# Kernel optimization log

Hardware: AMD Instinct MI355X
Metric: run time of the kernel (lower is better)

## Reference

```python
import jax, jax.numpy as jnp
import numpy as np

B, L, C = 8, 2048, 512
R, H, DK = 256, 8, 64
MASK_NEG = -2.0**15 + 1.0


def setup_inputs() -> dict:
    key = jax.random.key(0)
    ks = jax.random.split(key, 9)
    s = 1.0 / np.sqrt(C)
    return {
        "qx": jax.random.normal(ks[0], (B, L, C), jnp.float32),
        "kx": jax.random.normal(ks[1], (B, L, C), jnp.float32),
        "vx": jax.random.normal(ks[2], (B, L, C), jnp.float32),
        "addLoss": jnp.zeros((), jnp.float32),
        "maskPAD": jnp.ones((B, L, L), jnp.bool_),
        "Wp": jax.random.normal(ks[3], (R, C), jnp.float32) * s,
        "WQ": jax.random.normal(ks[4], (H * DK, C), jnp.float32) * s,
        "WK": jax.random.normal(ks[5], (H * DK, C), jnp.float32) * s,
        "WV": jax.random.normal(ks[6], (H * DK, C), jnp.float32) * s,
        "WO": jax.random.normal(ks[7], (C, H * DK), jnp.float32) * (1.0 / np.sqrt(H * DK)),
    }


def reference(qx, kx, vx, addLoss, maskPAD, Wp, WQ, WK, WV, WO):
    # linearLevel == 'l1', dropout treated as identity (eval), training losses included
    b, l, c = qx.shape
    r = Wp.shape[0]
    offI = (1.0 - jnp.eye(r, dtype=qx.dtype))  # ones_minus_I, [r, r]

    pScore = jnp.einsum('blc,rc->blr', vx, Wp)                       # [B, L, r]
    pad = (maskPAD[:, 0] == 0)                                       # [B, L]
    pScore = jnp.where(pad[:, :, None], MASK_NEG, pScore)
    pAlpha = jnp.swapaxes(jax.nn.softmax(pScore, axis=-2), -1, -2)   # [B, r, L]
    pAlpha_ = jax.nn.softmax(pScore, axis=-1)                        # [B, L, r]

    addLoss = addLoss + jnp.mean((jnp.einsum('brl,bsl->brs', pAlpha, pAlpha) * offI) ** 2)

    qr = pAlpha @ qx                                                 # [B, r, C]
    kr = pAlpha @ kx
    vr = pAlpha @ vx

    queries = (qr @ WQ.T).reshape(b, r, H, DK).transpose(0, 2, 1, 3)  # [B, H, r, dk]
    keys = (kr @ WK.T).reshape(b, r, H, DK).transpose(0, 2, 1, 3)
    values = (vr @ WV.T).reshape(b, r, H, DK).transpose(0, 2, 1, 3)

    scores = jnp.einsum('bhrd,bhsd->bhrs', queries, keys) / jnp.asarray(np.sqrt(DK), qx.dtype)
    alpha = jax.nn.softmax(scores, axis=-1)                          # [B, H, r, r]
    addLoss = addLoss + jnp.mean(alpha * offI)

    z = alpha @ values                                               # [B, H, r, dk]
    z = z.transpose(0, 2, 1, 3).reshape(b, r, H * DK)
    z = z @ WO.T                                                     # [B, r, C]

    addLoss = addLoss + jnp.mean((jnp.einsum('blr,bls->brs', pAlpha_, pAlpha_) * offI) ** 2)
    z = pAlpha_ @ z                                                  # [B, L, C]
    return z, scores, addLoss
```

## Files before the change

### kernel.cpp

```cpp
#include <hip/hip_runtime.h>

#define B_  8
#define L_  2048
#define C_  512
#define R_  256
#define H_  8
#define DK_ 64
#define HD_ 512
#define MASK_NEG (-32767.0f)

typedef __attribute__((ext_vector_type(8))) short short8;
typedef __attribute__((ext_vector_type(8))) unsigned short ushort8;
typedef __attribute__((ext_vector_type(4))) unsigned short ushort4_t;
typedef __attribute__((ext_vector_type(4))) float f32x4;
typedef unsigned short u16;

__device__ inline u16 bf16_rne(float x) {
    unsigned u = __float_as_uint(x);
    return (u16)((u + 0x7FFFu + ((u >> 16) & 1u)) >> 16);
}
__device__ inline unsigned cvt_hl(float x) {
    u16 hh = bf16_rne(x);
    float hf = __uint_as_float(((unsigned)hh) << 16);
    u16 ll = bf16_rne(x - hf);
    return (unsigned)hh | ((unsigned)ll << 16);
}

struct Ptr3 { const void* p0; const void* p1; const void* p2; };

#define GLL16(g, l) __builtin_amdgcn_global_load_lds( \
    (const __attribute__((address_space(1))) void*)(g), \
    (__attribute__((address_space(3))) void*)(l), 16, 0, 0)

template<int BN, int AMODE, int BMODE, int EPI, bool TRIPLE, int NTERM = 3, int KSPLIT = 1>
__global__ __launch_bounds__(256) void gemm_pl(
    Ptr3 aH, Ptr3 aL, Ptr3 bH, Ptr3 bL, Ptr3 cH, Ptr3 cL,
    Ptr3 cT1, Ptr3 cT2, int ldct, long long csT,
    int K, int lda, int ldb, int ldc, int divz,
    long long ash, long long bsh, long long csh,
    long long asb, long long bsb, long long csb,
    long long ksa, long long ksb, long long ksc,
    float scale)
{
    constexpr int NF = BN / 32;
    constexpr int XA = (NTERM == 3) ? 64 : 1;
    constexpr int XB = (NTERM == 3) ? BN : 1;
    __shared__ u16 Ahs[64][40], Als[XA][40];
    __shared__ u16 Bhs[BN][40], Bls[XB][40];

    const int gx = gridDim.x, gy = gridDim.y;
    const int nwg = gx * gy * gridDim.z;
    int flat = blockIdx.x + gx * (blockIdx.y + gy * blockIdx.z);
    {
        int q = nwg >> 3;
        int xcd = flat & 7, idx = flat >> 3;
        flat = xcd * q + idx;
    }
    const int bx = flat % gx;
    const int by = (flat / gx) % gy;
    const int z  = flat / (gx * gy);

    const int zb = z / divz;
    const int rem = z - zb * divz;
    const int zh = rem / KSPLIT, ks = rem - zh * KSPLIT;
    const int Keff = K / KSPLIT;
    const void* avH = TRIPLE ? (zb == 0 ? aH.p0 : zb == 1 ? aH.p1 : aH.p2) : aH.p0;
    const void* avL = TRIPLE ? (zb == 0 ? aL.p0 : zb == 1 ? aL.p1 : aL.p2) : aL.p0;
    const void* bvH = TRIPLE ? (zb == 0 ? bH.p0 : zb == 1 ? bH.p1 : bH.p2) : bH.p0;
    const void* bvL = TRIPLE ? (zb == 0 ? bL.p0 : zb == 1 ? bL.p1 : bL.p2) : bL.p0;
    void* cvH = (void*)(TRIPLE ? (zb == 0 ? cH.p0 : zb == 1 ? cH.p1 : cH.p2) : cH.p0);
    void* cvL = (void*)(TRIPLE ? (zb == 0 ? cL.p0 : zb == 1 ? cL.p1 : cL.p2) : cL.p0);
    void* cvT1 = (void*)(TRIPLE ? (zb == 0 ? cT1.p0 : zb == 1 ? cT1.p1 : cT1.p2) : cT1.p0);
    void* cvT2 = (void*)(TRIPLE ? (zb == 0 ? cT2.p0 : zb == 1 ? cT2.p1 : cT2.p2) : cT2.p0);
    const long long ao = (TRIPLE ? 0 : (long long)zb * asb) + (long long)zh * ash + (long long)ks * ksa;
    const long long bo = (TRIPLE ? 0 : (long long)zb * bsb) + (long long)zh * bsh + (long long)ks * ksb;
    const long long co = (TRIPLE ? 0 : (long long)zb * csb) + (long long)zh * csh + (long long)ks * ksc;
    const long long coT = (long long)zh * csT;

    const u16*   AHg = (const u16*)avH + ao;
    const u16*   ALg = (const u16*)avL + ao;
    const u16*   BHg = (const u16*)bvH + bo;
    const u16*   BLg = (const u16*)bvL + bo;
    const float* Bfg = (const float*)bvH + bo;
    float* Cf  = (float*)cvH + co;
    u16*   CHg = (u16*)cvH + co;
    u16*   CLg = (u16*)cvL + co;

    const int m0 = by * 64, n0 = bx * BN;
    const int tid = threadIdx.x;
    const int lane = tid & 63, w = tid >> 6;
    const int wrow = (w >> 1) * 32, wcol = (w & 1) * (BN / 2);
    const int l15 = lane & 15, lg = lane >> 4;

    f32x4 zero = {0.f, 0.f, 0.f, 0.f};
    f32x4 acc[2][NF];
    #pragma unroll
    for (int mf = 0; mf < 2; ++mf)
        #pragma unroll
        for (int nf = 0; nf < NF; ++nf) acc[mf][nf] = zero;

    for (int k0 = 0; k0 < Keff; k0 += 32) {
        {
            int row = tid >> 2, kc = (tid & 3) << 3;
            long long off = (long long)(m0 + row) * lda + (k0 + kc);
            *(ushort8*)&Ahs[row][kc] = *(const ushort8*)(AHg + off);
            if constexpr (NTERM == 3)
                *(ushort8*)&Als[row][kc] = *(const ushort8*)(ALg + off);
        }
        if (BMODE == 0) {
            #pragma unroll
            for (int t = tid; t < BN * 4; t += 256) {
                int row = t >> 2, kc = (t & 3) << 3;
                long long off = (long long)(n0 + row) * ldb + (k0 + kc);
                *(ushort8*)&Bhs[row][kc] = *(const ushort8*)(BHg + off);
                if constexpr (NTERM == 3)
                    *(ushort8*)&Bls[row][kc] = *(const ushort8*)(BLg + off);
            }
        } else {
            #pragma unroll
            for (int t = tid; t < BN * 4; t += 256) {
                int row = t >> 2, kc = (t & 3) << 3;
                const float* s = Bfg + (long long)(n0 + row) * ldb + (k0 + kc);
                float4 v0 = *(const float4*)s, v1 = *(const float4*)(s + 4);
                unsigned p0 = cvt_hl(v0.x), p1 = cvt_hl(v0.y), p2 = cvt_hl(v0.z), p3 = cvt_hl(v0.w);
                unsigned p4 = cvt_hl(v1.x), p5 = cvt_hl(v1.y), p6 = cvt_hl(v1.z), p7 = cvt_hl(v1.w);
                ushort8 h, l;
                h[0]=(u16)p0; h[1]=(u16)p1; h[2]=(u16)p2; h[3]=(u16)p3;
                h[4]=(u16)p4; h[5]=(u16)p5; h[6]=(u16)p6; h[7]=(u16)p7;
                l[0]=(u16)(p0>>16); l[1]=(u16)(p1>>16); l[2]=(u16)(p2>>16); l[3]=(u16)(p3>>16);
                l[4]=(u16)(p4>>16); l[5]=(u16)(p5>>16); l[6]=(u16)(p6>>16); l[7]=(u16)(p7>>16);
                *(ushort8*)&Bhs[row][kc] = h;
                if constexpr (NTERM == 3)
                    *(ushort8*)&Bls[row][kc] = l;
            }
        }
        __syncthreads();

        short8 a_h[2], a_l[2];
        a_h[0] = *(const short8*)&Ahs[wrow +      l15][lg * 8];
        a_h[1] = *(const short8*)&Ahs[wrow + 16 + l15][lg * 8];
        if constexpr (NTERM == 3) {
            a_l[0] = *(const short8*)&Als[wrow +      l15][lg * 8];
            a_l[1] = *(const short8*)&Als[wrow + 16 + l15][lg * 8];
        }
        #pragma unroll
        for (int nf = 0; nf < NF; ++nf) {
            short8 b_h = *(const short8*)&Bhs[wcol + nf * 16 + l15][lg * 8];
            if constexpr (NTERM == 3) {
                short8 b_l = *(const short8*)&Bls[wcol + nf * 16 + l15][lg * 8];
                #pragma unroll
                for (int mf = 0; mf < 2; ++mf) {
                    acc[mf][nf] = __builtin_amdgcn_mfma_f32_16x16x32_bf16(a_h[mf], b_h, acc[mf][nf], 0, 0, 0);
                    acc[mf][nf] = __builtin_amdgcn_mfma_f32_16x16x32_bf16(a_h[mf], b_l, acc[mf][nf], 0, 0, 0);
                    acc[mf][nf] = __builtin_amdgcn_mfma_f32_16x16x32_bf16(a_l[mf], b_h, acc[mf][nf], 0, 0, 0);
                }
            } else {
                #pragma unroll
                for (int mf = 0; mf < 2; ++mf)
                    acc[mf][nf] = __builtin_amdgcn_mfma_f32_16x16x32_bf16(a_h[mf], b_h, acc[mf][nf], 0, 0, 0);
            }
        }
        __syncthreads();
    }

    #pragma unroll
    for (int mf = 0; mf < 2; ++mf)
        #pragma unroll
        for (int nf = 0; nf < NF; ++nf) {
            int row = m0 + wrow + mf * 16 + lg * 4;
            int col = n0 + wcol + nf * 16 + l15;
            if constexpr (EPI == 0 || EPI == 3) {
                #pragma unroll
                for (int j = 0; j < 4; ++j)
                    Cf[(long long)(row + j) * ldc + col] = acc[mf][nf][j] * scale;
                if constexpr (EPI == 3) {
                    float* CfT = (float*)cvT1 + coT;
                    float4 v = make_float4(acc[mf][nf][0] * scale, acc[mf][nf][1] * scale,
                                           acc[mf][nf][2] * scale, acc[mf][nf][3] * scale);
                    *(float4*)(CfT + (long long)col * ldct + row) = v;
                }
            } else {
                unsigned p[4];
                #pragma unroll
                for (int j = 0; j < 4; ++j) {
                    p[j] = cvt_hl(acc[mf][nf][j] * scale);
                    if constexpr (EPI != 5) {
                        CHg[(long long)(row + j) * ldc + col] = (u16)p[j];
                        CLg[(long long)(row + j) * ldc + col] = (u16)(p[j] >> 16);
                    }
                }
                if constexpr (EPI == 4 || EPI == 5) {
                    u16* CTH = (u16*)cvT1 + coT;
                    u16* CTL = (u16*)cvT2 + coT;
                    ushort4_t h, l;
                    #pragma unroll
                    for (int j = 0; j < 4; ++j) { h[j] = (u16)p[j]; l[j] = (u16)(p[j] >> 16); }
                    *(ushort4_t*)(CTH + (long long)col * ldct + row) = h;
                    *(ushort4_t*)(CTL + (long long)col * ldct + row) = l;
                }
            }
        }
}

template<int EPI, bool TRIPLE, int NTERM, int KSPLIT, bool TRIANG = false>
__global__ __launch_bounds__(256) void gemm_gll(
    Ptr3 aH, Ptr3 aL, Ptr3 bH, Ptr3 bL, Ptr3 cH, Ptr3 cL,
    Ptr3 cT1, Ptr3 cT2, int ldct, long long csT,
    int K, int lda, int ldb, int ldc, int divz,
    long long ash, long long bsh, long long csh,
    long long ksa, long long ksb, long long ksc,
    float scale)
{
    constexpr int XA = (NTERM == 3) ? 128 : 1;
    __shared__ u16 Ahs[2][128][32];
    __shared__ u16 Bhs[2][128][32];
    __shared__ u16 Als[XA][32], Bls[XA][32];

    const int gx = gridDim.x, gy = gridDim.y;
    const int nwg = gx * gy * gridDim.z;
    int flat = blockIdx.x + gx * (blockIdx.y + gy * blockIdx.z);
    {
        int q = nwg >> 3;
        int xcd = flat & 7, idx = flat >> 3;
        flat = xcd * q + idx;
    }
    const int bx = flat % gx;
    const int by = (flat / gx) % gy;
    const int z  = flat / (gx * gy);

    const int zb = z / divz;
    const int rem = z - zb * divz;
    const int zh = rem / KSPLIT, ks = rem - zh * KSPLIT;
    const int Keff = K / KSPLIT;
    const void* avH = TRIPLE ? (zb == 0 ? aH.p0 : zb == 1 ? aH.p1 : aH.p2) : aH.p0;
    const void* avL = TRIPLE ? (zb == 0 ? aL.p0 : zb == 1 ? aL.p1 : aL.p2) : aL.p0;
    const void* bvH = TRIPLE ? (zb == 0 ? bH.p0 : zb == 1 ? bH.p1 : bH.p2) : bH.p0;
    const void* bvL = TRIPLE ? (zb == 0 ? bL.p0 : zb == 1 ? bL.p1 : bL.p2) : bL.p0;
    void* cvH = (void*)(TRIPLE ? (zb == 0 ? cH.p0 : zb == 1 ? cH.p1 : cH.p2) : cH.p0);
    void* cvL = (void*)(TRIPLE ? (zb == 0 ? cL.p0 : zb == 1 ? cL.p1 : cL.p2) : cL.p0);
    void* cvT1 = (void*)(TRIPLE ? (zb == 0 ? cT1.p0 : zb == 1 ? cT1.p1 : cT1.p2) : cT1.p0);
    void* cvT2 = (void*)(TRIPLE ? (zb == 0 ? cT2.p0 : zb == 1 ? cT2.p1 : cT2.p2) : cT2.p0);
    const long long ao = (long long)zh * ash + (long long)ks * ksa;
    const long long bo = (long long)zh * bsh + (long long)ks * ksb;
    const long long co = (long long)zh * csh + (long long)ks * ksc;
    const long long coT = (long long)zh * csT;

    const u16* AHg = (const u16*)avH + ao;
    const u16* ALg = (const u16*)avL + ao;
    const u16* BHg = (const u16*)bvH + bo;
    const u16* BLg = (const u16*)bvL + bo;
    float* Cf  = (float*)cvH + co;
    u16*   CHg = (u16*)cvH + co;
    u16*   CLg = (u16*)cvL + co;

    int m0, n0;
    if constexpr (TRIANG) {
        m0 = (bx >= 1) ? 128 : 0;
        n0 = (bx == 2) ? 128 : 0;
    } else {
        m0 = by * 128; n0 = bx * 128;
    }
    const int tid = threadIdx.x;
    const int lane = tid & 63, w = tid >> 6;
    const int wrow = (w >> 1) * 64, wcol = (w & 1) * 64;
    const int l15 = lane & 15, lg = lane >> 4;

    f32x4 zero = {0.f, 0.f, 0.f, 0.f};
    f32x4 acc[4][4];
    #pragma unroll
    for (int mf = 0; mf < 4; ++mf)
        #pragma unroll
        for (int nf = 0; nf < 4; ++nf) acc[mf][nf] = zero;

    const int ric = lane >> 2;
    const int cc  = lane & 3;

    auto STAGE_HI = [&](int bufsel, int k0) {
        #pragma unroll
        for (int i = 0; i < 2; ++i) {
            int chunk = w * 2 + i;
            int row = chunk * 16 + ric;
            int gcol = ((cc ^ ((row >> 1) & 3)) << 3);
            GLL16(AHg + (long long)(m0 + row) * lda + (k0 + gcol), &Ahs[bufsel][chunk * 16][0]);
            GLL16(BHg + (long long)(n0 + row) * ldb + (k0 + gcol), &Bhs[bufsel][chunk * 16][0]);
        }
    };
    auto STAGE_LO = [&](int k0) {
        #pragma unroll
        for (int i = 0; i < 2; ++i) {
            int chunk = w * 2 + i;
            int row = chunk * 16 + ric;
            int gcol = ((cc ^ ((row >> 1) & 3)) << 3);
            GLL16(ALg + (long long)(m0 + row) * lda + (k0 + gcol), &Als[chunk * 16][0]);
            GLL16(BLg + (long long)(n0 + row) * ldb + (k0 + gcol), &Bls[chunk * 16][0]);
        }
    };

    const int nt = Keff / 32;
    int cur = 0;
    STAGE_HI(0, 0);

    for (int t = 0; t < nt; ++t) {
        if constexpr (NTERM == 3) STAGE_LO(t * 32);
        if (t + 1 < nt) {
            STAGE_HI(cur ^ 1, (t + 1) * 32);
            asm volatile("s_waitcnt vmcnt(4)" ::: "memory");
        } else {
            asm volatile("s_waitcnt vmcnt(0)" ::: "memory");
        }
        __builtin_amdgcn_s_barrier();

        short8 a_h[4], a_l[4];
        #pragma unroll
        for (int mf = 0; mf < 4; ++mf) {
            int ar = wrow + mf * 16 + l15;
            int ac = (lg ^ ((ar >> 1) & 3)) << 3;
            a_h[mf] = *(const short8*)&Ahs[cur][ar][ac];
            if constexpr (NTERM == 3) a_l[mf] = *(const short8*)&Als[ar][ac];
        }
        __builtin_amdgcn_s_setprio(1);
        #pragma unroll
        for (int nf = 0; nf < 4; ++nf) {
            int br = wcol + nf * 16 + l15;
            int bc = (lg ^ ((br >> 1) & 3)) << 3;
            short8 b_h = *(const short8*)&Bhs[cur][br][bc];
            if constexpr (NTERM == 3) {
                short8 b_l = *(const short8*)&Bls[br][bc];
                #pragma unroll
                for (int mf = 0; mf < 4; ++mf) {
                    acc[mf][nf] = __builtin_amdgcn_mfma_f32_16x16x32_bf16(a_h[mf], b_h, acc[mf][nf], 0, 0, 0);
                    acc[mf][nf] = __builtin_amdgcn_mfma_f32_16x16x32_bf16(a_h[mf], b_l, acc[mf][nf], 0, 0, 0);
                    acc[mf][nf] = __builtin_amdgcn_mfma_f32_16x16x32_bf16(a_l[mf], b_h, acc[mf][nf], 0, 0, 0);
                }
            } else {
                #pragma unroll
                for (int mf = 0; mf < 4; ++mf)
                    acc[mf][nf] = __builtin_amdgcn_mfma_f32_16x16x32_bf16(a_h[mf], b_h, acc[mf][nf], 0, 0, 0);
            }
        }
        __builtin_amdgcn_s_setprio(0);
        __builtin_amdgcn_s_barrier();
        cur ^= 1;
    }

    #pragma unroll
    for (int mf = 0; mf < 4; ++mf)
        #pragma unroll
        for (int nf = 0; nf < 4; ++nf) {
            int row = m0 + wrow + mf * 16 + lg * 4;
            int col = n0 + wcol + nf * 16 + l15;
            if constexpr (EPI == 0) {
                #pragma unroll
                for (int j = 0; j < 4; ++j)
                    Cf[(long long)(row + j) * ldc + col] = acc[mf][nf][j] * scale;
            } else {
                unsigned p[4];
                #pragma unroll
                for (int j = 0; j < 4; ++j) {
                    p[j] = cvt_hl(acc[mf][nf][j] * scale);
                    CHg[(long long)(row + j) * ldc + col] = (u16)p[j];
                    CLg[(long long)(row + j) * ldc + col] = (u16)(p[j] >> 16);
                }
                if constexpr (EPI == 3) {
                    if (cvT1) {
                        u16* CTH = (u16*)cvT1 + coT;
                        u16* CTL = (u16*)cvT2 + coT;
                        ushort4_t h, l;
                        #pragma unroll
                        for (int j = 0; j < 4; ++j) { h[j] = (u16)p[j]; l[j] = (u16)(p[j] >> 16); }
                        *(ushort4_t*)(CTH + (long long)col * ldct + row) = h;
                        *(ushort4_t*)(CTL + (long long)col * ldct + row) = l;
                    }
                }
            }
        }
}

#define KS_ 4
__global__ __launch_bounds__(256) void loss_reduce2(
    const float* __restrict__ G1, const float* __restrict__ G2,
    int nks, float* __restrict__ lossBase)
{
    __shared__ float red[4];
    const long long N = (long long)B_ * R_ * R_;
    int seg = blockIdx.x >> 9;
    const float* G = seg ? G2 : G1;
    float* lossDst = lossBase + (seg ? 2 : 0);
    long long i4 = ((long long)(blockIdx.x & 511) * 256 + threadIdx.x) << 2;
    float s = 0.0f;
    if (i4 < N) {
        int e = (int)(i4 & (long long)(R_ * R_ - 1));
        int row = e >> 8, c0 = e & 255;
        if (!(row < 128 && c0 >= 128)) {
            float4 g = make_float4(0.f, 0.f, 0.f, 0.f);
            for (int ks = 0; ks < nks; ++ks) {
                float4 v = *(const float4*)(G + (long long)ks * N + i4);
                g.x += v.x; g.y += v.y; g.z += v.z; g.w += v.w;
            }
            float wgt = (row >= 128 && c0 < 128) ? 2.0f : 1.0f;
            if (row != c0 + 0) s += wgt * g.x * g.x;
            if (row != c0 + 1) s += wgt * g.y * g.y;
            if (row != c0 + 2) s += wgt * g.z * g.z;
            if (row != c0 + 3) s += wgt * g.w * g.w;
        }
    }
    #pragma unroll
    for (int o = 32; o; o >>= 1) s += __shfl_down(s, o, 64);
    int lane = threadIdx.x & 63, wid = threadIdx.x >> 6;
    if (lane == 0) red[wid] = s;
    __syncthreads();
    if (threadIdx.x == 0) atomicAdd(lossDst, red[0] + red[1] + red[2] + red[3]);
}

#define NKS6_ 2
__global__ __launch_bounds__(256) void qkv_reduce(
    const float* __restrict__ Cpart, Ptr3 dstH, Ptr3 dstL)
{
    const long long T = (long long)B_ * R_ * C_;
    long long i4 = (long long)blockIdx.x * 256 + threadIdx.x;
    if (i4 >= 3 * (T >> 2)) return;
    int member = (int)(i4 / (T >> 2));
    long long rem = (i4 - (long long)member * (T >> 2)) << 2;
    float4 a = *(const float4*)(Cpart + (long long)member * T + rem);
    #pragma unroll
    for (int ks = 1; ks < NKS6_; ++ks) {
        float4 b = *(const float4*)(Cpart + (long long)ks * 3 * T + (long long)member * T + rem);
        a.x += b.x; a.y += b.y; a.z += b.z; a.w += b.w;
    }
    unsigned q0 = cvt_hl(a.x), q1 = cvt_hl(a.y), q2 = cvt_hl(a.z), q3 = cvt_hl(a.w);
    ushort4_t h, l;
    h[0]=(u16)q0; h[1]=(u16)q1; h[2]=(u16)q2; h[3]=(u16)q3;
    l[0]=(u16)(q0>>16); l[1]=(u16)(q1>>16); l[2]=(u16)(q2>>16); l[3]=(u16)(q3>>16);
    u16* dH = (u16*)(member == 0 ? dstH.p0 : member == 1 ? dstH.p1 : dstH.p2);
    u16* dL = (u16*)(member == 0 ? dstL.p0 : member == 1 ? dstL.p1 : dstL.p2);
    *(ushort4_t*)(dH + rem) = h;
    *(ushort4_t*)(dL + rem) = l;
}

__global__ __launch_bounds__(256) void xpose_f32p3(
    Ptr3 src, Ptr3 dstH, Ptr3 dstL,
    int M, int N, long long ibs, long long obs, int divz)
{
    __shared__ float S[64][65];
    int z = blockIdx.z;
    int m = z / divz, b = z - m * divz;
    const float* ip = (const float*)(m == 0 ? src.p0 : m == 1 ? src.p1 : src.p2)
                      + (long long)b * ibs;
    u16* opH = (u16*)(m == 0 ? dstH.p0 : m == 1 ? dstH.p1 : dstH.p2) + (long long)b * obs;
    u16* opL = (u16*)(m == 0 ? dstL.p0 : m == 1 ? dstL.p1 : dstL.p2) + (long long)b * obs;
    int n0 = blockIdx.x * 64, m0 = blockIdx.y * 64;
    int t = threadIdx.x;
    int c4 = (t & 15) << 2, rq = t >> 4;
    #pragma unroll
    for (int p = 0; p < 4; ++p) {
        int r = p * 16 + rq;
        float4 v = *(const float4*)(ip + (long long)(m0 + r) * N + n0 + c4);
        S[r][c4+0]=v.x; S[r][c4+1]=v.y; S[r][c4+2]=v.z; S[r][c4+3]=v.w;
    }
    __syncthreads();
    #pragma unroll
    for (int p = 0; p < 4; ++p) {
        int nr = p * 16 + rq;
        unsigned q0 = cvt_hl(S[c4+0][nr]), q1 = cvt_hl(S[c4+1][nr]);
        unsigned q2 = cvt_hl(S[c4+2][nr]), q3 = cvt_hl(S[c4+3][nr]);
        ushort4_t h, l;
        h[0]=(u16)q0; h[1]=(u16)q1; h[2]=(u16)q2; h[3]=(u16)q3;
        l[0]=(u16)(q0>>16); l[1]=(u16)(q1>>16); l[2]=(u16)(q2>>16); l[3]=(u16)(q3>>16);
        long long ob = (long long)(n0 + nr) * M + m0 + c4;
        *(ushort4_t*)(opH + ob) = h;
        *(ushort4_t*)(opL + ob) = l;
    }
}

__global__ __launch_bounds__(256) void xpose_u16p(
    const u16* __restrict__ inH, const u16* __restrict__ inL,
    u16* __restrict__ outH, u16* __restrict__ outL,
    int M, int N, long long ibs, long long obs)
{
    __shared__ u16 SH[64][66], SL[64][66];
    const u16* ipH = inH + (long long)blockIdx.z * ibs;
    const u16* ipL = inL + (long long)blockIdx.z * ibs;
    u16* opH = outH + (long long)blockIdx.z * obs;
    u16* opL = outL + (long long)blockIdx.z * obs;
    int n0 = blockIdx.x * 64, m0 = blockIdx.y * 64;
    int t = threadIdx.x;
    int c4 = (t & 15) << 2, rq = t >> 4;
    #pragma unroll
    for (int p = 0; p < 4; ++p) {
        int r = p * 16 + rq;
        long long ib = (long long)(m0 + r) * N + n0 + c4;
        ushort4_t vh = *(const ushort4_t*)(ipH + ib);
        ushort4_t vl = *(const ushort4_t*)(ipL + ib);
        SH[r][c4+0]=vh[0]; SH[r][c4+1]=vh[1]; SH[r][c4+2]=vh[2]; SH[r][c4+3]=vh[3];
        SL[r][c4+0]=vl[0]; SL[r][c4+1]=vl[1]; SL[r][c4+2]=vl[2]; SL[r][c4+3]=vl[3];
    }
    __syncthreads();
    #pragma unroll
    for (int p = 0; p < 4; ++p) {
        int nr = p * 16 + rq;
        ushort4_t h, l;
        h[0]=SH[c4+0][nr]; h[1]=SH[c4+1][nr]; h[2]=SH[c4+2][nr]; h[3]=SH[c4+3][nr];
        l[0]=SL[c4+0][nr]; l[1]=SL[c4+1][nr]; l[2]=SL[c4+2][nr]; l[3]=SL[c4+3][nr];
        long long ob = (long long)(n0 + nr) * M + m0 + c4;
        *(ushort4_t*)(opH + ob) = h;
        *(ushort4_t*)(opL + ob) = l;
    }
}

__device__ inline float waveMax(float v) {
    #pragma unroll
    for (int o = 32; o; o >>= 1) v = fmaxf(v, __shfl_xor(v, o, 64));
    return v;
}
__device__ inline float waveSum(float v) {
    #pragma unroll
    for (int o = 32; o; o >>= 1) v += __shfl_xor(v, o, 64);
    return v;
}

__global__ __launch_bounds__(256) void conv_planes5(
    const float* __restrict__ s0, const float* __restrict__ s1, const float* __restrict__ s2,
    const float* __restrict__ s3, const float* __restrict__ s4,
    u16* h0, u16* l0, u16* h1, u16* l1, u16* h2, u16* l2,
    u16* h3, u16* l3, u16* h4, u16* l4)
{
    const int N0 = 32768, NW = 65536;
    int i = blockIdx.x * 256 + threadIdx.x;
    if (i >= N0 + 4 * NW) return;
    const float* s; u16* h; u16* l; int off;
    if (i < N0) { s = s0; h = h0; l = l0; off = i; }
    else {
        int j = i - N0, seg = j / NW;
        off = j - seg * NW;
        s = seg == 0 ? s1 : seg == 1 ? s2 : seg == 2 ? s3 : s4;
        h = seg == 0 ? h1 : seg == 1 ? h2 : seg == 2 ? h3 : h4;
        l = seg == 0 ? l1 : seg == 1 ? l2 : seg == 2 ? l3 : l4;
    }
    float4 v = ((const float4*)s)[off];
    unsigned p0 = cvt_hl(v.x), p1 = cvt_hl(v.y), p2 = cvt_hl(v.z), p3 = cvt_hl(v.w);
    ushort4_t hv, lv;
    hv[0]=(u16)p0; hv[1]=(u16)p1; hv[2]=(u16)p2; hv[3]=(u16)p3;
    lv[0]=(u16)(p0>>16); lv[1]=(u16)(p1>>16); lv[2]=(u16)(p2>>16); lv[3]=(u16)(p3>>16);
    ((ushort4_t*)h)[off] = hv;
    ((ushort4_t*)l)[off] = lv;
}

__global__ __launch_bounds__(256) void softmax_both(
    const float* __restrict__ pT, const float* __restrict__ pScore,
    const int* __restrict__ mask,
    u16* __restrict__ ltH, u16* __restrict__ ltL,
    u16* __restrict__ rH, u16* __restrict__ rL)
{
    __shared__ float sm[4], ss[4];
    int bxid = blockIdx.x;
    int lane = threadIdx.x & 63, wid = threadIdx.x >> 6;
    if (bxid < B_ * R_) {
        int zi = bxid;
        int b = zi >> 8;
        const float* row = pT + (long long)zi * L_;
        const int* mk = mask + (long long)b * L_ * L_;
        float vals[8];
        float mx = -3.4e38f;
        #pragma unroll
        for (int i = 0; i < 8; ++i) {
            int l = threadIdx.x + i * 256;
            float v = row[l];
            if (mk[l] == 0) v = MASK_NEG;
            vals[i] = v; mx = fmaxf(mx, v);
        }
        mx = waveMax(mx);
        if (lane == 0) sm[wid] = mx;
        __syncthreads();
        mx = fmaxf(fmaxf(sm[0], sm[1]), fmaxf(sm[2], sm[3]));
        float sum = 0.0f;
        #pragma unroll
        for (int i = 0; i < 8; ++i) { float e = __expf(vals[i] - mx); vals[i] = e; sum += e; }
        sum = waveSum(sum);
        if (lane == 0) ss[wid] = sum;
        __syncthreads();
        sum = ss[0] + ss[1] + ss[2] + ss[3];
        float inv = 1.0f / sum;
        long long base = (long long)zi * L_;
        #pragma unroll
        for (int i = 0; i < 8; ++i) {
            unsigned p = cvt_hl(vals[i] * inv);
            ltH[base + threadIdx.x + i * 256] = (u16)p;
            ltL[base + threadIdx.x + i * 256] = (u16)(p >> 16);
        }
    } else {
        long long z = (long long)(bxid - B_ * R_) * 4 + wid;
        int b = (int)(z >> 11), l = (int)(z & 2047);
        bool pad = (mask[(long long)b * L_ * L_ + l] == 0);
        float4 v = *(const float4*)(pScore + z * R_ + lane * 4);
        if (pad) { v.x = MASK_NEG; v.y = MASK_NEG; v.z = MASK_NEG; v.w = MASK_NEG; }
        float mx = waveMax(fmaxf(fmaxf(v.x, v.y), fmaxf(v.z, v.w)));
        float e0 = __expf(v.x - mx), e1 = __expf(v.y - mx);
        float e2 = __expf(v.z - mx), e3 = __expf(v.w - mx);
        float inv = 1.0f / waveSum(e0 + e1 + e2 + e3);
        unsigned p0 = cvt_hl(e0 * inv), p1 = cvt_hl(e1 * inv);
        unsigned p2 = cvt_hl(e2 * inv), p3 = cvt_hl(e3 * inv);
        ushort4_t h, lo;
        h[0]=(u16)p0; h[1]=(u16)p1; h[2]=(u16)p2; h[3]=(u16)p3;
        lo[0]=(u16)(p0>>16); lo[1]=(u16)(p1>>16); lo[2]=(u16)(p2>>16); lo[3]=(u16)(p3>>16);
        *(ushort4_t*)(rH + z * R_ + lane * 4) = h;
        *(ushort4_t*)(rL + z * R_ + lane * 4) = lo;
    }
}

__global__ __launch_bounds__(256) void softmax_alpha4(
    const float* __restrict__ scores, u16* __restrict__ aH, u16* __restrict__ aL,
    float* __restrict__ offArr)
{
    int lane = threadIdx.x & 63, wid = threadIdx.x >> 6;
    long long row = (long long)blockIdx.x * 4 + wid;
    int r = (int)(row & 255);
    float4 v = *(const float4*)(scores + row * 256 + lane * 4);
    float mx = waveMax(fmaxf(fmaxf(v.x, v.y), fmaxf(v.z, v.w)));
    float e0 = __expf(v.x - mx), e1 = __expf(v.y - mx);
    float e2 = __expf(v.z - mx), e3 = __expf(v.w - mx);
    float inv = 1.0f / waveSum(e0 + e1 + e2 + e3);
    float a0 = e0 * inv, a1 = e1 * inv, a2 = e2 * inv, a3 = e3 * inv;
    unsigned p0 = cvt_hl(a0), p1 = cvt_hl(a1), p2 = cvt_hl(a2), p3 = cvt_hl(a3);
    ushort4_t h, lo;
    h[0]=(u16)p0; h[1]=(u16)p1; h[2]=(u16)p2; h[3]=(u16)p3;
    lo[0]=(u16)(p0>>16); lo[1]=(u16)(p1>>16); lo[2]=(u16)(p2>>16); lo[3]=(u16)(p3>>16);
    *(ushort4_t*)(aH + row * 256 + lane * 4) = h;
    *(ushort4_t*)(aL + row * 256 + lane * 4) = lo;
    int c = lane * 4;
    float off = (c + 0 == r ? 0.0f : a0) + (c + 1 == r ? 0.0f : a1)
              + (c + 2 == r ? 0.0f : a2) + (c + 3 == r ? 0.0f : a3);
    off = waveSum(off);
    if (lane == 0) offArr[row] = off;
}

__global__ __launch_bounds__(256) void finalize_loss(
    const float* __restrict__ addLossIn, const float* __restrict__ lossAcc,
    const float* __restrict__ offArr, float* __restrict__ out)
{
    __shared__ float red[4];
    float s = 0.0f;
    for (int i = threadIdx.x; i < B_ * H_ * R_; i += 256) s += offArr[i];
    int lane = threadIdx.x & 63, wid = threadIdx.x >> 6;
    s = waveSum(s);
    if (lane == 0) red[wid] = s;
    __syncthreads();
    if (threadIdx.x == 0) {
        float total = red[0] + red[1] + red[2] + red[3];
        out[0] = addLossIn[0]
               + lossAcc[0] * (1.0f / ((float)B_ * R_ * R_))
               + total      * (1.0f / ((float)B_ * H_ * R_ * R_))
               + lossAcc[2] * (1.0f / ((float)B_ * R_ * R_));
    }
}

extern "C" void kernel_launch(void* const* d_in, const int* in_sizes, int n_in,
                              void* d_out, int out_size, void* d_ws, size_t ws_size,
                              hipStream_t stream)
{
    const float* qx = (const float*)d_in[0];
    const float* kx = (const float*)d_in[1];
    const float* vx = (const float*)d_in[2];
    const float* addLossIn = (const float*)d_in[3];
    const int* mask = (const int*)d_in[4];
    const float* Wp = (const float*)d_in[5];
    const float* WQ = (const float*)d_in[6];
    const float* WK = (const float*)d_in[7];
    const float* WV = (const float*)d_in[8];
    const float* WO = (const float*)d_in[9];

    float* zOut      = (float*)d_out;
    float* scoresOut = zOut + (long long)B_ * L_ * C_;
    float* lossOut   = scoresOut + (long long)B_ * H_ * R_ * R_;

    const long long S = (long long)B_ * L_ * R_;
    const long long T = (long long)B_ * R_ * C_;
    u16* cur = (u16*)d_ws;
    auto takeU = [&](long long n) { u16* p = cur; cur += n; return p; };
    auto takeF = [&](long long n) { float* p = (float*)cur; cur += 2 * n; return p; };

    float* pScore   = takeF(S);
    float* pScoreT  = takeF(S);
    u16* pAlphaH  = takeU(S);
    u16* pAlphaL  = takeU(S);
    u16* pAlpha_H = takeU(S);
    u16* pAlpha_L = takeU(S);
    u16* pATH     = takeU(S);
    u16* pATL     = takeU(S);
    u16* xTH0 = takeU(2*S); u16* xTL0 = takeU(2*S);
    u16* xTH1 = takeU(2*S); u16* xTL1 = takeU(2*S);
    u16* xTH2 = takeU(2*S); u16* xTL2 = takeU(2*S);
    const long long llRR = (long long)R_ * R_;
    float* Gpart  = takeF(2LL * KS_ * B_ * llRR);
    float* Cpart6 = takeF((long long)NKS6_ * 3 * T);
    u16* qrH = takeU(T); u16* qrL = takeU(T);
    u16* krH = takeU(T); u16* krL = takeU(T);
    u16* vrH = takeU(T); u16* vrL = takeU(T);
    u16* qpH = takeU(T); u16* qpL = takeU(T);
    u16* kpH = takeU(T); u16* kpL = takeU(T);
    u16* vpH = takeU(T); u16* vpL = takeU(T);
    u16* vpTH = takeU(T); u16* vpTL = takeU(T);
    u16* z1H = takeU(T); u16* z1L = takeU(T);
    u16* z2TH = takeU(T); u16* z2TL = takeU(T);
    u16* alphaH = takeU(S); u16* alphaL = takeU(S);
    u16* WpH = takeU((long long)R_ * C_); u16* WpL = takeU((long long)R_ * C_);
    u16* WQH = takeU((long long)HD_ * C_); u16* WQL = takeU((long long)HD_ * C_);
    u16* WKH = takeU((long long)HD_ * C_); u16* WKL = takeU((long long)HD_ * C_);
    u16* WVH = takeU((long long)HD_ * C_); u16* WVL = takeU((long long)HD_ * C_);
    u16* WOH = takeU((long long)HD_ * C_); u16* WOL = takeU((long long)HD_ * C_);
    float* loss   = takeF(16);
    float* offArr = takeF(B_ * H_ * R_);

    const Ptr3 N3{nullptr, nullptr, nullptr};
    auto P1 = [](const void* p) { return Ptr3{p, p, p}; };
    const long long llRL = (long long)R_ * L_, llLC = (long long)L_ * C_;
    const long long llRC = (long long)R_ * C_, llRHD = (long long)R_ * HD_;
    const long long llHRR = (long long)H_ * R_ * R_;
    const long long llCL = (long long)C_ * L_;
    float* Gpart2 = Gpart + (long long)KS_ * B_ * llRR;

    (void)hipMemsetAsync(loss, 0, 3 * sizeof(float), stream);

    conv_planes5<<<1152, 256, 0, stream>>>(
        Wp, WQ, WK, WV, WO,
        WpH, WpL, WQH, WQL, WKH, WKL, WVH, WVL, WOH, WOL);

    gemm_pl<64, 0, 2, 3, false><<<dim3(L_/64, R_/64, B_), 256, 0, stream>>>(
        P1(WpH), P1(WpL), P1(vx), N3, P1(pScoreT), N3,
        P1(pScore), N3, R_, llRL,
        C_, C_, C_, L_, B_,
        0, llLC, llRL, 0, 0, 0, 0, 0, 0, 1.0f);

    softmax_both<<<B_ * R_ + B_ * L_ / 4, 256, 0, stream>>>(
        pScoreT, pScore, mask, pAlphaH, pAlphaL, pAlpha_H, pAlpha_L);

    xpose_u16p<<<dim3(R_/64, L_/64, B_), 256, 0, stream>>>(
        pAlpha_H, pAlpha_L, pATH, pATL, L_, R_, llRL, llRL);

    gemm_gll<0, true, 1, KS_, true><<<dim3(3, 1, 2 * B_ * KS_), 256, 0, stream>>>(
        Ptr3{pAlphaH, pATH, pATH}, N3, Ptr3{pAlphaH, pATH, pATH}, N3,
        Ptr3{Gpart, Gpart2, Gpart2}, N3,
        N3, N3, 0, 0,
        L_, L_, L_, R_, B_ * KS_,
        llRL, llRL, llRR,
        L_ / KS_, L_ / KS_, (long long)B_ * llRR, 1.0f);
    loss_reduce2<<<1024, 256, 0, stream>>>(Gpart, Gpart2, KS_, loss);

    xpose_f32p3<<<dim3(C_/64, L_/64, 3 * B_), 256, 0, stream>>>(
        Ptr3{qx, kx, vx}, Ptr3{xTH0, xTH1, xTH2}, Ptr3{xTL0, xTL1, xTL2},
        L_, C_, llLC, llCL, B_);

    gemm_gll<0, true, 3, NKS6_><<<dim3(C_/128, R_/128, 3 * B_ * NKS6_), 256, 0, stream>>>(
        P1(pAlphaH), P1(pAlphaL),
        Ptr3{xTH0, xTH1, xTH2}, Ptr3{xTL0, xTL1, xTL2},
        Ptr3{Cpart6, Cpart6 + T, Cpart6 + 2 * T}, N3,
        N3, N3, 0, 0,
        L_, L_, L_, C_, B_ * NKS6_,
        llRL, llCL, llRC,
        L_ / NKS6_, L_ / NKS6_, 3 * T, 1.0f);

    qkv_reduce<<<(int)(3 * (T >> 2) / 256), 256, 0, stream>>>(
        Cpart6, Ptr3{qrH, krH, vrH}, Ptr3{qrL, krL, vrL});

    gemm_gll<3, true, 3, 1><<<dim3(HD_/128, 2, 3 * B_), 256, 0, stream>>>(
        Ptr3{qrH, krH, vrH}, Ptr3{qrL, krL, vrL},
        Ptr3{WQH, WKH, WVH}, Ptr3{WQL, WKL, WVL},
        Ptr3{qpH, kpH, vpH}, Ptr3{qpL, kpL, vpL},
        Ptr3{nullptr, nullptr, vpTH}, Ptr3{nullptr, nullptr, vpTL}, R_, llRHD,
        C_, C_, C_, HD_, B_,
        llRC, 0, llRHD,
        0, 0, 0, 1.0f);

    gemm_pl<64, 0, 0, 0, false><<<dim3(4, 4, 64), 256, 0, stream>>>(
        P1(qpH), P1(qpL), P1(kpH), P1(kpL), P1(scoresOut), N3,
        N3, N3, 0, 0,
        DK_, HD_, HD_, R_, 8, 64, 64, llRR, llRHD, llRHD, llHRR,
        0, 0, 0, 0.125f);

    softmax_alpha4<<<B_ * H_ * R_ / 4, 256, 0, stream>>>(scoresOut, alphaH, alphaL, offArr);

    gemm_pl<64, 0, 0, 2, false><<<dim3(1, 4, 64), 256, 0, stream>>>(
        P1(alphaH), P1(alphaL), P1(vpTH), P1(vpTL), P1(z1H), P1(z1L),
        N3, N3, 0, 0,
        R_, R_, R_, HD_, 8, llRR, (long long)64 * R_, 64, llHRR, llRHD, llRHD,
        0, 0, 0, 1.0f);

    gemm_pl<64, 0, 0, 5, false><<<dim3(HD_/64, R_/64, B_), 256, 0, stream>>>(
        P1(z1H), P1(z1L), P1(WOH), P1(WOL), N3, N3,
        P1(z2TH), P1(z2TL), R_, llRC,
        HD_, HD_, HD_, C_, B_,
        llRHD, 0, llRC, 0, 0, 0, 0, 0, 0, 1.0f);

    gemm_gll<0, false, 3, 1><<<dim3(C_/128, L_/128, B_), 256, 0, stream>>>(
        P1(pAlpha_H), P1(pAlpha_L), P1(z2TH), P1(z2TL), P1(zOut), N3,
        N3, N3, 0, 0,
        R_, R_, R_, C_, B_,
        llRL, llRC, llLC,
        0, 0, 0, 1.0f);

    finalize_loss<<<1, 256, 0, stream>>>(addLossIn, loss, offArr, lossOut);
}
```

Baseline: 307.1 us.

## Fuse pAlpha_ transpose into softmax and drop split-K for qkv reduction GEMM

```diff
diff --git a/kernel.cpp b/kernel.cpp
--- a/kernel.cpp
+++ b/kernel.cpp
@@ -412,31 +412,6 @@
     if (threadIdx.x == 0) atomicAdd(lossDst, red[0] + red[1] + red[2] + red[3]);
 }
 
-#define NKS6_ 2
-__global__ __launch_bounds__(256) void qkv_reduce(
-    const float* __restrict__ Cpart, Ptr3 dstH, Ptr3 dstL)
-{
-    const long long T = (long long)B_ * R_ * C_;
-    long long i4 = (long long)blockIdx.x * 256 + threadIdx.x;
-    if (i4 >= 3 * (T >> 2)) return;
-    int member = (int)(i4 / (T >> 2));
-    long long rem = (i4 - (long long)member * (T >> 2)) << 2;
-    float4 a = *(const float4*)(Cpart + (long long)member * T + rem);
-    #pragma unroll
-    for (int ks = 1; ks < NKS6_; ++ks) {
-        float4 b = *(const float4*)(Cpart + (long long)ks * 3 * T + (long long)member * T + rem);
-        a.x += b.x; a.y += b.y; a.z += b.z; a.w += b.w;
-    }
-    unsigned q0 = cvt_hl(a.x), q1 = cvt_hl(a.y), q2 = cvt_hl(a.z), q3 = cvt_hl(a.w);
-    ushort4_t h, l;
-    h[0]=(u16)q0; h[1]=(u16)q1; h[2]=(u16)q2; h[3]=(u16)q3;
-    l[0]=(u16)(q0>>16); l[1]=(u16)(q1>>16); l[2]=(u16)(q2>>16); l[3]=(u16)(q3>>16);
-    u16* dH = (u16*)(member == 0 ? dstH.p0 : member == 1 ? dstH.p1 : dstH.p2);
-    u16* dL = (u16*)(member == 0 ? dstL.p0 : member == 1 ? dstL.p1 : dstL.p2);
-    *(ushort4_t*)(dH + rem) = h;
-    *(ushort4_t*)(dL + rem) = l;
-}
-
 __global__ __launch_bounds__(256) void xpose_f32p3(
     Ptr3 src, Ptr3 dstH, Ptr3 dstL,
     int M, int N, long long ibs, long long obs, int divz)
@@ -466,41 +441,6 @@
         ushort4_t h, l;
         h[0]=(u16)q0; h[1]=(u16)q1; h[2]=(u16)q2; h[3]=(u16)q3;
         l[0]=(u16)(q0>>16); l[1]=(u16)(q1>>16); l[2]=(u16)(q2>>16); l[3]=(u16)(q3>>16);
-        long long ob = (long long)(n0 + nr) * M + m0 + c4;
-        *(ushort4_t*)(opH + ob) = h;
-        *(ushort4_t*)(opL + ob) = l;
-    }
-}
-
-__global__ __launch_bounds__(256) void xpose_u16p(
-    const u16* __restrict__ inH, const u16* __restrict__ inL,
-    u16* __restrict__ outH, u16* __restrict__ outL,
-    int M, int N, long long ibs, long long obs)
-{
-    __shared__ u16 SH[64][66], SL[64][66];
-    const u16* ipH = inH + (long long)blockIdx.z * ibs;
-    const u16* ipL = inL + (long long)blockIdx.z * ibs;
-    u16* opH = outH + (long long)blockIdx.z * obs;
-    u16* opL = outL + (long long)blockIdx.z * obs;
-    int n0 = blockIdx.x * 64, m0 = blockIdx.y * 64;
-    int t = threadIdx.x;
-    int c4 = (t & 15) << 2, rq = t >> 4;
-    #pragma unroll
-    for (int p = 0; p < 4; ++p) {
-        int r = p * 16 + rq;
-        long long ib = (long long)(m0 + r) * N + n0 + c4;
-        ushort4_t vh = *(const ushort4_t*)(ipH + ib);
-        ushort4_t vl = *(const ushort4_t*)(ipL + ib);
-        SH[r][c4+0]=vh[0]; SH[r][c4+1]=vh[1]; SH[r][c4+2]=vh[2]; SH[r][c4+3]=vh[3];
-        SL[r][c4+0]=vl[0]; SL[r][c4+1]=vl[1]; SL[r][c4+2]=vl[2]; SL[r][c4+3]=vl[3];
-    }
-    __syncthreads();
-    #pragma unroll
-    for (int p = 0; p < 4; ++p) {
-        int nr = p * 16 + rq;
-        ushort4_t h, l;
-        h[0]=SH[c4+0][nr]; h[1]=SH[c4+1][nr]; h[2]=SH[c4+2][nr]; h[3]=SH[c4+3][nr];
-        l[0]=SL[c4+0][nr]; l[1]=SL[c4+1][nr]; l[2]=SL[c4+2][nr]; l[3]=SL[c4+3][nr];
         long long ob = (long long)(n0 + nr) * M + m0 + c4;
         *(ushort4_t*)(opH + ob) = h;
         *(ushort4_t*)(opL + ob) = l;
@@ -549,9 +489,11 @@
     const float* __restrict__ pT, const float* __restrict__ pScore,
     const int* __restrict__ mask,
     u16* __restrict__ ltH, u16* __restrict__ ltL,
-    u16* __restrict__ rH, u16* __restrict__ rL)
+    u16* __restrict__ rH, u16* __restrict__ rL,
+    u16* __restrict__ patH, u16* __restrict__ patL)
 {
     __shared__ float sm[4], ss[4];
+    __shared__ unsigned P32[256][65];
     int bxid = blockIdx.x;
     int lane = threadIdx.x & 63, wid = threadIdx.x >> 6;
     if (bxid < B_ * R_) {
@@ -588,22 +530,47 @@
             ltL[base + threadIdx.x + i * 256] = (u16)(p >> 16);
         }
     } else {
-        long long z = (long long)(bxid - B_ * R_) * 4 + wid;
-        int b = (int)(z >> 11), l = (int)(z & 2047);
-        bool pad = (mask[(long long)b * L_ * L_ + l] == 0);
-        float4 v = *(const float4*)(pScore + z * R_ + lane * 4);
-        if (pad) { v.x = MASK_NEG; v.y = MASK_NEG; v.z = MASK_NEG; v.w = MASK_NEG; }
-        float mx = waveMax(fmaxf(fmaxf(v.x, v.y), fmaxf(v.z, v.w)));
-        float e0 = __expf(v.x - mx), e1 = __expf(v.y - mx);
-        float e2 = __expf(v.z - mx), e3 = __expf(v.w - mx);
-        float inv = 1.0f / waveSum(e0 + e1 + e2 + e3);
-        unsigned p0 = cvt_hl(e0 * inv), p1 = cvt_hl(e1 * inv);
-        unsigned p2 = cvt_hl(e2 * inv), p3 = cvt_hl(e3 * inv);
-        ushort4_t h, lo;
-        h[0]=(u16)p0; h[1]=(u16)p1; h[2]=(u16)p2; h[3]=(u16)p3;
-        lo[0]=(u16)(p0>>16); lo[1]=(u16)(p1>>16); lo[2]=(u16)(p2>>16); lo[3]=(u16)(p3>>16);
-        *(ushort4_t*)(rH + z * R_ + lane * 4) = h;
-        *(ushort4_t*)(rL + z * R_ + lane * 4) = lo;
+        int bid2 = bxid - B_ * R_;
+        int b = (bid2 * 64) >> 11;
+        int l0 = (bid2 * 64) & 2047;
+        const long long mrow = (long long)b * L_ * L_;
+        #pragma unroll
+        for (int j = 0; j < 16; ++j) {
+            int rr = wid * 16 + j;
+            long long z = (long long)bid2 * 64 + rr;
+            bool pad = (mask[mrow + l0 + rr] == 0);
+            float4 v = *(const float4*)(pScore + z * R_ + lane * 4);
+            if (pad) { v.x = MASK_NEG; v.y = MASK_NEG; v.z = MASK_NEG; v.w = MASK_NEG; }
+            float mx = waveMax(fmaxf(fmaxf(v.x, v.y), fmaxf(v.z, v.w)));
+            float e0 = __expf(v.x - mx), e1 = __expf(v.y - mx);
+            float e2 = __expf(v.z - mx), e3 = __expf(v.w - mx);
+            float inv = 1.0f / waveSum(e0 + e1 + e2 + e3);
+            unsigned p0 = cvt_hl(e0 * inv), p1 = cvt_hl(e1 * inv);
+            unsigned p2 = cvt_hl(e2 * inv), p3 = cvt_hl(e3 * inv);
+            ushort4_t h, lo;
+            h[0]=(u16)p0; h[1]=(u16)p1; h[2]=(u16)p2; h[3]=(u16)p3;
+            lo[0]=(u16)(p0>>16); lo[1]=(u16)(p1>>16); lo[2]=(u16)(p2>>16); lo[3]=(u16)(p3>>16);
+            *(ushort4_t*)(rH + z * R_ + lane * 4) = h;
+            *(ushort4_t*)(rL + z * R_ + lane * 4) = lo;
+            P32[lane * 4 + 0][rr] = p0;
+            P32[lane * 4 + 1][rr] = p1;
+            P32[lane * 4 + 2][rr] = p2;
+            P32[lane * 4 + 3][rr] = p3;
+        }
+        __syncthreads();
+        int r = threadIdx.x;
+        long long ob = (long long)b * ((long long)R_ * L_) + (long long)r * L_ + l0;
+        #pragma unroll
+        for (int c = 0; c < 8; ++c) {
+            ushort8 h8, l8;
+            #pragma unroll
+            for (int i = 0; i < 8; ++i) {
+                unsigned p = P32[r][c * 8 + i];
+                h8[i] = (u16)p; l8[i] = (u16)(p >> 16);
+            }
+            *(ushort8*)(patH + ob + c * 8) = h8;
+            *(ushort8*)(patL + ob + c * 8) = l8;
+        }
     }
 }
 
@@ -691,7 +658,6 @@
     u16* xTH2 = takeU(2*S); u16* xTL2 = takeU(2*S);
     const long long llRR = (long long)R_ * R_;
     float* Gpart  = takeF(2LL * KS_ * B_ * llRR);
-    float* Cpart6 = takeF((long long)NKS6_ * 3 * T);
     u16* qrH = takeU(T); u16* qrL = takeU(T);
     u16* krH = takeU(T); u16* krL = takeU(T);
     u16* vrH = takeU(T); u16* vrL = takeU(T);
@@ -730,11 +696,8 @@
         C_, C_, C_, L_, B_,
         0, llLC, llRL, 0, 0, 0, 0, 0, 0, 1.0f);
 
-    softmax_both<<<B_ * R_ + B_ * L_ / 4, 256, 0, stream>>>(
-        pScoreT, pScore, mask, pAlphaH, pAlphaL, pAlpha_H, pAlpha_L);
-
-    xpose_u16p<<<dim3(R_/64, L_/64, B_), 256, 0, stream>>>(
-        pAlpha_H, pAlpha_L, pATH, pATL, L_, R_, llRL, llRL);
+    softmax_both<<<B_ * R_ + B_ * L_ / 64, 256, 0, stream>>>(
+        pScoreT, pScore, mask, pAlphaH, pAlphaL, pAlpha_H, pAlpha_L, pATH, pATL);
 
     gemm_gll<0, true, 1, KS_, true><<<dim3(3, 1, 2 * B_ * KS_), 256, 0, stream>>>(
         Ptr3{pAlphaH, pATH, pATH}, N3, Ptr3{pAlphaH, pATH, pATH}, N3,
@@ -749,17 +712,14 @@
         Ptr3{qx, kx, vx}, Ptr3{xTH0, xTH1, xTH2}, Ptr3{xTL0, xTL1, xTL2},
         L_, C_, llLC, llCL, B_);
 
-    gemm_gll<0, true, 3, NKS6_><<<dim3(C_/128, R_/128, 3 * B_ * NKS6_), 256, 0, stream>>>(
+    gemm_gll<2, true, 3, 1><<<dim3(C_/128, R_/128, 3 * B_), 256, 0, stream>>>(
         P1(pAlphaH), P1(pAlphaL),
         Ptr3{xTH0, xTH1, xTH2}, Ptr3{xTL0, xTL1, xTL2},
-        Ptr3{Cpart6, Cpart6 + T, Cpart6 + 2 * T}, N3,
+        Ptr3{qrH, krH, vrH}, Ptr3{qrL, krL, vrL},
         N3, N3, 0, 0,
-        L_, L_, L_, C_, B_ * NKS6_,
+        L_, L_, L_, C_, B_,
         llRL, llCL, llRC,
-        L_ / NKS6_, L_ / NKS6_, 3 * T, 1.0f);
-
-    qkv_reduce<<<(int)(3 * (T >> 2) / 256), 256, 0, stream>>>(
-        Cpart6, Ptr3{qrH, krH, vrH}, Ptr3{qrL, krL, vrL});
+        0, 0, 0, 1.0f);
 
     gemm_gll<3, true, 3, 1><<<dim3(HD_/128, 2, 3 * B_), 256, 0, stream>>>(
         Ptr3{qrH, krH, vrH}, Ptr3{qrL, krL, vrL},
```

Result: slower. 334.7 us (+9.0%).
